# Kernel tuning notes

Hardware: AMD Instinct MI355X
Metric: run time of the kernel (lower is better)

## Reference

```python
import jax, jax.numpy as jnp
import numpy as np

E = 1024   # embed_size
H = 16     # num_heads
D = E // H # head_dim
B, S = 4, 2048

def setup_inputs() -> dict:
    key = jax.random.key(0)
    ks = jax.random.split(key, 11)
    scale = 1.0 / np.sqrt(E)
    inp = {
        "Q": jax.random.normal(ks[0], (B, S, E), jnp.float32),
        "K": jax.random.normal(ks[1], (B, S, E), jnp.float32),
        "V": jax.random.normal(ks[2], (B, S, E), jnp.float32),
        "Wq": jax.random.uniform(ks[3], (E, E), jnp.float32, -scale, scale),
        "bq": jax.random.uniform(ks[4], (E,), jnp.float32, -scale, scale),
        "Wk": jax.random.uniform(ks[5], (E, E), jnp.float32, -scale, scale),
        "bk": jax.random.uniform(ks[6], (E,), jnp.float32, -scale, scale),
        "Wv": jax.random.uniform(ks[7], (E, E), jnp.float32, -scale, scale),
        "bv": jax.random.uniform(ks[8], (E,), jnp.float32, -scale, scale),
        "Wo": jax.random.uniform(ks[9], (E, E), jnp.float32, -scale, scale),
        "bo": jax.random.uniform(ks[10], (E,), jnp.float32, -scale, scale),
    }
    return inp

def reference(Q, K, V, Wq, bq, Wk, bk, Wv, bv, Wo, bo):
    b, sq, _ = Q.shape
    sk = K.shape[1]
    # Linear projections (torch Linear: x @ W.T + b), split into heads -> (b, H, s, D)
    q = (Q @ Wq.T + bq).reshape(b, sq, H, D).transpose(0, 2, 1, 3)
    k = (K @ Wk.T + bk).reshape(b, sk, H, D).transpose(0, 2, 1, 3)
    v = (V @ Wv.T + bv).reshape(b, sk, H, D).transpose(0, 2, 1, 3)
    scores = jnp.einsum('bhqd,bhkd->bhqk', q, k) / jnp.sqrt(jnp.float32(D))
    attn = jax.nn.softmax(scores, axis=-1)
    out = jnp.einsum('bhqk,bhkd->bhqd', attn, v)  # (b, H, sq, D)
    concat = out.transpose(0, 2, 1, 3).reshape(b, sq, E)
    return concat @ Wo.T + bo
```

## Files before the change

### kernel.cpp

```cpp
#include <hip/hip_runtime.h>
#include <hip/hip_bf16.h>

typedef unsigned short u16;
typedef unsigned int u32;
typedef __bf16 bf16x8 __attribute__((ext_vector_type(8)));
typedef float f32x4 __attribute__((ext_vector_type(4)));
typedef float f32x16 __attribute__((ext_vector_type(16)));
typedef unsigned int u32x2 __attribute__((ext_vector_type(2)));

constexpr int E_ = 1024, H_ = 16, D_ = 64, B_ = 4, S_ = 2048;
constexpr int GM = B_ * S_;
constexpr int GN = E_;
constexpr int GK = E_;

__device__ __forceinline__ u16 f2bf(float f) {
  union { float f; u32 u; } v; v.f = f;
  u32 r = v.u + 0x7fffu + ((v.u >> 16) & 1u);
  return (u16)(r >> 16);
}

__device__ __forceinline__ bf16x8 ld_bf16x8(const u16* p) {
  return *reinterpret_cast<const bf16x8*>(p);
}

__device__ __forceinline__ f32x4 mfma16(bf16x8 a, bf16x8 b, f32x4 c) {
  return __builtin_amdgcn_mfma_f32_16x16x32_bf16(a, b, c, 0, 0, 0);
}
__device__ __forceinline__ f32x16 mfma32(bf16x8 a, bf16x8 b, f32x16 c) {
  return __builtin_amdgcn_mfma_f32_32x32x16_bf16(a, b, c, 0, 0, 0);
}

__device__ __forceinline__ u32 cvtpk(float lo, float hi) {
  u32 r;
  asm("v_cvt_pk_bf16_f32 %0, %1, %2" : "=v"(r) : "v"(lo), "v"(hi));
  return r;
}

__device__ __forceinline__ void pl32swap(u32& a, u32& b) {
#if __has_builtin(__builtin_amdgcn_permlane32_swap)
  u32x2 r = __builtin_amdgcn_permlane32_swap(a, b, false, false);
  a = r.x; b = r.y;
#else
  asm volatile("v_permlane32_swap_b32 %0, %1" : "+v"(a), "+v"(b));
#endif
}

__device__ __forceinline__ float fexp2(float x) {
#if __has_builtin(__builtin_amdgcn_exp2f)
  return __builtin_amdgcn_exp2f(x);
#else
  return exp2f(x);
#endif
}

#define GLOAD_LDS16(gp, lp)                                                       \
  __builtin_amdgcn_global_load_lds(                                               \
      (const __attribute__((address_space(1))) u32*)(const void*)(gp),            \
      (__attribute__((address_space(3))) u32*)(void*)(lp), 16, 0, 0)

__global__ __launch_bounds__(256) void cvt7(
    const float4* __restrict__ s0, const float4* __restrict__ s1,
    const float4* __restrict__ s2, const float4* __restrict__ s3,
    const float4* __restrict__ s4, const float4* __restrict__ s5,
    const float4* __restrict__ s6,
    ushort4* __restrict__ d0, ushort4* __restrict__ d1,
    ushort4* __restrict__ d2, ushort4* __restrict__ d3,
    ushort4* __restrict__ d4, ushort4* __restrict__ d5,
    ushort4* __restrict__ d6) {
  long i = (long)blockIdx.x * 256 + threadIdx.x;
  const float4* s; ushort4* d; long j;
  if (i < 2097152L)      { s = s0; d = d0; j = i; }
  else if (i < 4194304L) { s = s1; d = d1; j = i - 2097152L; }
  else if (i < 6291456L) { s = s2; d = d2; j = i - 4194304L; }
  else if (i < 6553600L) { s = s3; d = d3; j = i - 6291456L; }
  else if (i < 6815744L) { s = s4; d = d4; j = i - 6553600L; }
  else if (i < 7077888L) { s = s5; d = d5; j = i - 6815744L; }
  else                   { s = s6; d = d6; j = i - 7077888L; }
  float4 v = s[j];
  ushort4 o;
  o.x = f2bf(v.x); o.y = f2bf(v.y); o.z = f2bf(v.z); o.w = f2bf(v.w);
  d[j] = o;
}

template <int MODE>
__global__ __launch_bounds__(256, 2) void gemm_bt(
    const u16* __restrict__ A, const u16* __restrict__ Bw,
    const float* __restrict__ bias, void* __restrict__ Cout, float scale) {
  __shared__ u16 As[128 * 32];
  __shared__ u16 Bs[128 * 32];
  const int tid = threadIdx.x;
  const int lane = tid & 63, w = tid >> 6;
  const int lr = lane & 15, lg = lane >> 4;
  const int bn = blockIdx.x, bm = blockIdx.y;
  const int wm = (w >> 1) * 64, wn = (w & 1) * 64;

  f32x4 acc[4][4] = {};

  const int byte0 = (w * 2 + 0) * 1024 + lane * 16;
  const int byte1 = (w * 2 + 1) * 1024 + lane * 16;
  const int r0 = byte0 >> 6, c0 = (byte0 & 63) >> 1;
  const int r1 = byte1 >> 6, c1 = (byte1 & 63) >> 1;
  const u16* Arow0 = A + (size_t)(bm * 128 + r0) * GK + c0;
  const u16* Arow1 = A + (size_t)(bm * 128 + r1) * GK + c1;
  const u16* Brow0 = Bw + (size_t)(bn * 128 + r0) * GK + c0;
  const u16* Brow1 = Bw + (size_t)(bn * 128 + r1) * GK + c1;
  u16* As0 = &As[(w * 2 + 0) * 512];
  u16* As1 = &As[(w * 2 + 1) * 512];
  u16* Bs0 = &Bs[(w * 2 + 0) * 512];
  u16* Bs1 = &Bs[(w * 2 + 1) * 512];

  for (int kt = 0; kt < GK / 32; ++kt) {
    const int ko = kt * 32;
    GLOAD_LDS16(Arow0 + ko, As0);
    GLOAD_LDS16(Arow1 + ko, As1);
    GLOAD_LDS16(Brow0 + ko, Bs0);
    GLOAD_LDS16(Brow1 + ko, Bs1);
    __syncthreads();
    bf16x8 af[4], bf_[4];
#pragma unroll
    for (int mi = 0; mi < 4; ++mi)
      af[mi] = ld_bf16x8(&As[(wm + mi * 16 + lr) * 32 + lg * 8]);
#pragma unroll
    for (int ni = 0; ni < 4; ++ni)
      bf_[ni] = ld_bf16x8(&Bs[(wn + ni * 16 + lr) * 32 + lg * 8]);
#pragma unroll
    for (int mi = 0; mi < 4; ++mi)
#pragma unroll
      for (int ni = 0; ni < 4; ++ni)
        acc[mi][ni] = mfma16(af[mi], bf_[ni], acc[mi][ni]);
    __syncthreads();
  }

#pragma unroll
  for (int mi = 0; mi < 4; ++mi)
#pragma unroll
    for (int ni = 0; ni < 4; ++ni) {
      const int n = bn * 128 + wn + ni * 16 + lr;
      const float bv = bias[n];
#pragma unroll
      for (int r = 0; r < 4; ++r) {
        const int m = bm * 128 + wm + mi * 16 + lg * 4 + r;
        const float vv = (acc[mi][ni][r] + bv) * scale;
        if (MODE == 0) {
          const int b = m >> 11, s = m & 2047, h = n >> 6, d = n & 63;
          ((u16*)Cout)[(((size_t)(b * 16 + h) * 2048 + s) * 64) + d] = f2bf(vv);
        } else if (MODE == 1) {
          const int b = m >> 11, s = m & 2047, h = n >> 6, d = n & 63;
          ((u16*)Cout)[((size_t)(b * 16 + h) * 64 + d) * 2048 + s] = f2bf(vv);
        } else {
          ((float*)Cout)[(size_t)m * 1024 + n] = vv;
        }
      }
    }
}

__global__ __launch_bounds__(256, 2) void attn5(
    const u16* __restrict__ q, const u16* __restrict__ k,
    const u16* __restrict__ vT, u16* __restrict__ concat) {
  __shared__ u16 KT[2][64 * 64];
  __shared__ u16 VTl[2][64 * 64];
  const int tid = threadIdx.x, lane = tid & 63, w = tid >> 6;
  const int l31 = lane & 31, hi = lane >> 5;
  const int bid = blockIdx.x;
  const int flat = (bid & 7) * 64 + (bid >> 3);
  const int bh = flat >> 3, qt = flat & 7;
  const u16* qbp = q + (size_t)bh * S_ * D_;
  const char* kbase = (const char*)(k + (size_t)bh * S_ * D_);
  const char* vbase = (const char*)(vT + (size_t)bh * D_ * S_);
  const int q0 = qt * 256 + w * 64;

  bf16x8 qf[2][4];
#pragma unroll
  for (int qs = 0; qs < 2; ++qs)
#pragma unroll
    for (int kc = 0; kc < 4; ++kc)
      qf[qs][kc] =
          ld_bf16x8(&qbp[(size_t)(q0 + qs * 32 + l31) * 64 + kc * 16 + hi * 8]);

  f32x16 acc[2][2] = {};
  float l_[2] = {0.f, 0.f};

  const int srow = w * 8 + (lane >> 3);
  const int cswz = (((lane & 7) ^ (lane >> 3)) << 4);
  const char* gk0 = kbase + (size_t)srow * 128 + cswz;
  const char* gk1 = kbase + (size_t)(32 + srow) * 128 + cswz;
  const char* gv0 = vbase + (size_t)srow * (S_ * 2) + cswz;
  const char* gv1 = vbase + (size_t)(32 + srow) * (S_ * 2) + cswz;

  int col4[4];
#pragma unroll
  for (int c = 0; c < 4; ++c)
    col4[c] = (((c * 32 + hi * 16) ^ ((lane & 7) << 4)) >> 1);
  const int rrow = l31 * 64;

#define STAGE(t, buf)                                                     \
  do {                                                                    \
    GLOAD_LDS16(gk0 + (size_t)(t) * 8192, &KT[buf][(0 * 4 + w) * 512]);   \
    GLOAD_LDS16(gk1 + (size_t)(t) * 8192, &KT[buf][(1 * 4 + w) * 512]);   \
    GLOAD_LDS16(gv0 + (size_t)(t) * 128, &VTl[buf][(0 * 4 + w) * 512]);   \
    GLOAD_LDS16(gv1 + (size_t)(t) * 128, &VTl[buf][(1 * 4 + w) * 512]);   \
  } while (0)

  STAGE(0, 0);
  asm volatile("s_waitcnt vmcnt(0)" ::: "memory");
  __syncthreads();

  for (int t = 0; t < S_ / 64; ++t) {
    const int cur = t & 1, nxt = cur ^ 1;
    if (t < S_ / 64 - 1) STAGE(t + 1, nxt);

    f32x16 sF[2][2] = {};
#pragma unroll
    for (int st = 0; st < 2; ++st)
#pragma unroll
      for (int kc = 0; kc < 4; ++kc) {
        bf16x8 kf = ld_bf16x8(&KT[cur][st * 2048 + rrow + col4[kc]]);
        sF[0][st] = mfma32(kf, qf[0][kc], sF[0][st]);
        sF[1][st] = mfma32(kf, qf[1][kc], sF[1][st]);
      }

    bf16x8 vt[2][4];
#pragma unroll
    for (int ks = 0; ks < 4; ++ks) {
      vt[0][ks] = ld_bf16x8(&VTl[cur][rrow + col4[ks]]);
      vt[1][ks] = ld_bf16x8(&VTl[cur][2048 + rrow + col4[ks]]);
    }

#pragma unroll
    for (int qs = 0; qs < 2; ++qs) {
      float s0 = 0.f, s1 = 0.f, s2 = 0.f, s3 = 0.f;
#pragma unroll
      for (int st = 0; st < 2; ++st)
#pragma unroll
        for (int e = 0; e < 16; e += 4) {
          const float p0 = fexp2(sF[qs][st][e + 0]);
          const float p1 = fexp2(sF[qs][st][e + 1]);
          const float p2 = fexp2(sF[qs][st][e + 2]);
          const float p3 = fexp2(sF[qs][st][e + 3]);
          sF[qs][st][e + 0] = p0; sF[qs][st][e + 1] = p1;
          sF[qs][st][e + 2] = p2; sF[qs][st][e + 3] = p3;
          s0 += p0; s1 += p1; s2 += p2; s3 += p3;
        }
      l_[qs] += (s0 + s1) + (s2 + s3);

#pragma unroll
      for (int ks = 0; ks < 4; ++ks) {
        const int st = ks >> 1, b = (ks & 1) * 8;
        u32 w0 = cvtpk(sF[qs][st][b + 0], sF[qs][st][b + 1]);
        u32 w1 = cvtpk(sF[qs][st][b + 2], sF[qs][st][b + 3]);
        u32 w2 = cvtpk(sF[qs][st][b + 4], sF[qs][st][b + 5]);
        u32 w3 = cvtpk(sF[qs][st][b + 6], sF[qs][st][b + 7]);
        pl32swap(w0, w2);
        pl32swap(w1, w3);
        union { u32 u[4]; bf16x8 v; } pa;
        pa.u[0] = w0; pa.u[1] = w1; pa.u[2] = w2; pa.u[3] = w3;
        acc[qs][0] = mfma32(vt[0][ks], pa.v, acc[qs][0]);
        acc[qs][1] = mfma32(vt[1][ks], pa.v, acc[qs][1]);
      }
    }

    asm volatile("s_waitcnt vmcnt(0)" ::: "memory");
    __syncthreads();
  }
#undef STAGE

  const int b = bh >> 4, h = bh & 15;
#pragma unroll
  for (int qs = 0; qs < 2; ++qs) {
    u32 la = __builtin_bit_cast(u32, l_[qs]), lb = la;
    pl32swap(la, lb);
    const float lt =
        __builtin_bit_cast(float, la) + __builtin_bit_cast(float, lb);
    const float inv = 1.f / lt;
    const int s = q0 + qs * 32 + l31;
    u16* crow = concat + ((size_t)(b * 2048 + s)) * 1024 + h * 64;
#pragma unroll
    for (int dt = 0; dt < 2; ++dt)
#pragma unroll
      for (int g = 0; g < 4; ++g) {
        ushort4 o;
        o.x = f2bf(acc[qs][dt][g * 4 + 0] * inv);
        o.y = f2bf(acc[qs][dt][g * 4 + 1] * inv);
        o.z = f2bf(acc[qs][dt][g * 4 + 2] * inv);
        o.w = f2bf(acc[qs][dt][g * 4 + 3] * inv);
        *(ushort4*)&crow[dt * 32 + g * 8 + hi * 4] = o;
      }
  }
}

extern "C" void kernel_launch(void* const* d_in, const int* in_sizes, int n_in,
                              void* d_out, int out_size, void* d_ws,
                              size_t ws_size, hipStream_t stream) {
  const float* Qf = (const float*)d_in[0];
  const float* Kf = (const float*)d_in[1];
  const float* Vf = (const float*)d_in[2];
  const float* Wq = (const float*)d_in[3];
  const float* bq = (const float*)d_in[4];
  const float* Wk = (const float*)d_in[5];
  const float* bk = (const float*)d_in[6];
  const float* Wv = (const float*)d_in[7];
  const float* bv = (const float*)d_in[8];
  const float* Wo = (const float*)d_in[9];
  const float* bo = (const float*)d_in[10];

  char* ws = (char*)d_ws;
  u16* Xq = (u16*)(ws);
  u16* Xk = Xq + 8388608;
  u16* Xv = Xk + 8388608;
  u16* Wqb = (u16*)(ws + (size_t)3 * 16777216);
  u16* Wkb = Wqb + 1048576;
  u16* Wvb = Wkb + 1048576;
  u16* Wob = Wvb + 1048576;
  u16* qb = (u16*)(ws + (size_t)3 * 16777216 + 8388608);
  u16* kb = qb + (size_t)GM * GN;
  u16* vTb = kb + (size_t)GM * GN;
  u16* concat = Xq;

  cvt7<<<28672, 256, 0, stream>>>(
      (const float4*)Qf, (const float4*)Kf, (const float4*)Vf,
      (const float4*)Wq, (const float4*)Wk, (const float4*)Wv,
      (const float4*)Wo, (ushort4*)Xq, (ushort4*)Xk, (ushort4*)Xv,
      (ushort4*)Wqb, (ushort4*)Wkb, (ushort4*)Wvb, (ushort4*)Wob);

  dim3 gg(GN / 128, GM / 128);
  gemm_bt<0><<<gg, 256, 0, stream>>>(Xq, Wqb, bq, qb, 0.18033688011112042f);
  gemm_bt<0><<<gg, 256, 0, stream>>>(Xk, Wkb, bk, kb, 1.0f);
  gemm_bt<1><<<gg, 256, 0, stream>>>(Xv, Wvb, bv, vTb, 1.0f);

  attn5<<<512, 256, 0, stream>>>(qb, kb, vTb, concat);

  gemm_bt<2><<<gg, 256, 0, stream>>>(concat, Wob, bo, (void*)d_out, 1.0f);
}
```

Before: 221.9 us.

## Double attention block to 8 waves and compute softmax row sums via MFMA

The attention kernel now runs 512 threads per block, with each block covering 512 queries of a head, so each K/V tile staged in shared memory is reused by twice as many waves and global loads per query drop. The exp row-sum moves from scalar adds plus a cross-lane swap onto an extra MFMA against a ones vector, which offloads VALU work to the matrix cores. The cost is half as many blocks (less parallelism across CUs), an extra MFMA per step, and denominators summed from bf16-rounded probabilities.

```diff
diff --git a/kernel.cpp b/kernel.cpp
--- a/kernel.cpp
+++ b/kernel.cpp
@@ -154,7 +154,7 @@
     }
 }
 
-__global__ __launch_bounds__(256, 2) void attn5(
+__global__ __launch_bounds__(512, 2) void attn7(
     const u16* __restrict__ q, const u16* __restrict__ k,
     const u16* __restrict__ vT, u16* __restrict__ concat) {
   __shared__ u16 KT[2][64 * 64];
@@ -162,12 +162,12 @@
   const int tid = threadIdx.x, lane = tid & 63, w = tid >> 6;
   const int l31 = lane & 31, hi = lane >> 5;
   const int bid = blockIdx.x;
-  const int flat = (bid & 7) * 64 + (bid >> 3);
-  const int bh = flat >> 3, qt = flat & 7;
+  const int flat = (bid & 7) * 32 + (bid >> 3);
+  const int bh = flat >> 2, qt = flat & 3;
   const u16* qbp = q + (size_t)bh * S_ * D_;
   const char* kbase = (const char*)(k + (size_t)bh * S_ * D_);
   const char* vbase = (const char*)(vT + (size_t)bh * D_ * S_);
-  const int q0 = qt * 256 + w * 64;
+  const int q0 = qt * 512 + w * 64;
 
   bf16x8 qf[2][4];
 #pragma unroll
@@ -178,14 +178,14 @@
           ld_bf16x8(&qbp[(size_t)(q0 + qs * 32 + l31) * 64 + kc * 16 + hi * 8]);
 
   f32x16 acc[2][2] = {};
-  float l_[2] = {0.f, 0.f};
-
-  const int srow = w * 8 + (lane >> 3);
-  const int cswz = (((lane & 7) ^ (lane >> 3)) << 4);
-  const char* gk0 = kbase + (size_t)srow * 128 + cswz;
-  const char* gk1 = kbase + (size_t)(32 + srow) * 128 + cswz;
-  const char* gv0 = vbase + (size_t)srow * (S_ * 2) + cswz;
-  const char* gv1 = vbase + (size_t)(32 + srow) * (S_ * 2) + cswz;
+  f32x16 accl[2] = {};
+  union { u32 u[4]; bf16x8 v; } ones_;
+  ones_.u[0] = ones_.u[1] = ones_.u[2] = ones_.u[3] = 0x3F803F80u;
+
+  const int srow = tid >> 3;
+  const int csw = ((tid & 7) ^ (srow & 7)) << 4;
+  const char* gk = kbase + (size_t)srow * 128 + csw;
+  const char* gv = vbase + (size_t)srow * 4096 + csw;
 
   int col4[4];
 #pragma unroll
@@ -193,12 +193,10 @@
     col4[c] = (((c * 32 + hi * 16) ^ ((lane & 7) << 4)) >> 1);
   const int rrow = l31 * 64;
 
-#define STAGE(t, buf)                                                     \
-  do {                                                                    \
-    GLOAD_LDS16(gk0 + (size_t)(t) * 8192, &KT[buf][(0 * 4 + w) * 512]);   \
-    GLOAD_LDS16(gk1 + (size_t)(t) * 8192, &KT[buf][(1 * 4 + w) * 512]);   \
-    GLOAD_LDS16(gv0 + (size_t)(t) * 128, &VTl[buf][(0 * 4 + w) * 512]);   \
-    GLOAD_LDS16(gv1 + (size_t)(t) * 128, &VTl[buf][(1 * 4 + w) * 512]);   \
+#define STAGE(t, buf)                                            \
+  do {                                                           \
+    GLOAD_LDS16(gk + (size_t)(t) * 8192, &KT[buf][tid * 8]);     \
+    GLOAD_LDS16(gv + (size_t)(t) * 128, &VTl[buf][tid * 8]);     \
   } while (0)
 
   STAGE(0, 0);
@@ -228,20 +226,10 @@
 
 #pragma unroll
     for (int qs = 0; qs < 2; ++qs) {
-      float s0 = 0.f, s1 = 0.f, s2 = 0.f, s3 = 0.f;
 #pragma unroll
       for (int st = 0; st < 2; ++st)
 #pragma unroll
-        for (int e = 0; e < 16; e += 4) {
-          const float p0 = fexp2(sF[qs][st][e + 0]);
-          const float p1 = fexp2(sF[qs][st][e + 1]);
-          const float p2 = fexp2(sF[qs][st][e + 2]);
-          const float p3 = fexp2(sF[qs][st][e + 3]);
-          sF[qs][st][e + 0] = p0; sF[qs][st][e + 1] = p1;
-          sF[qs][st][e + 2] = p2; sF[qs][st][e + 3] = p3;
-          s0 += p0; s1 += p1; s2 += p2; s3 += p3;
-        }
-      l_[qs] += (s0 + s1) + (s2 + s3);
+        for (int e = 0; e < 16; ++e) sF[qs][st][e] = fexp2(sF[qs][st][e]);
 
 #pragma unroll
       for (int ks = 0; ks < 4; ++ks) {
@@ -256,6 +244,7 @@
         pa.u[0] = w0; pa.u[1] = w1; pa.u[2] = w2; pa.u[3] = w3;
         acc[qs][0] = mfma32(vt[0][ks], pa.v, acc[qs][0]);
         acc[qs][1] = mfma32(vt[1][ks], pa.v, acc[qs][1]);
+        accl[qs] = mfma32(ones_.v, pa.v, accl[qs]);
       }
     }
 
@@ -267,11 +256,7 @@
   const int b = bh >> 4, h = bh & 15;
 #pragma unroll
   for (int qs = 0; qs < 2; ++qs) {
-    u32 la = __builtin_bit_cast(u32, l_[qs]), lb = la;
-    pl32swap(la, lb);
-    const float lt =
-        __builtin_bit_cast(float, la) + __builtin_bit_cast(float, lb);
-    const float inv = 1.f / lt;
+    const float inv = 1.f / accl[qs][0];
     const int s = q0 + qs * 32 + l31;
     u16* crow = concat + ((size_t)(b * 2048 + s)) * 1024 + h * 64;
 #pragma unroll
@@ -327,7 +312,7 @@
   gemm_bt<0><<<gg, 256, 0, stream>>>(Xk, Wkb, bk, kb, 1.0f);
   gemm_bt<1><<<gg, 256, 0, stream>>>(Xv, Wvb, bv, vTb, 1.0f);
 
-  attn5<<<512, 256, 0, stream>>>(qb, kb, vTb, concat);
+  attn7<<<256, 512, 0, stream>>>(qb, kb, vTb, concat);
 
   gemm_bt<2><<<gg, 256, 0, stream>>>(concat, Wob, bo, (void*)d_out, 1.0f);
 }
```

New measurement: 222.8 us. No clear change (+0.4%).

## Load K and V tiles directly from global memory, dropping LDS staging

Applied to the files above, without the earlier changes.

The attention kernel stops staging K and V^T tiles through double-buffered shared memory with async global-to-LDS loads and block barriers. Each wave now reads its MFMA operands straight from global memory, relying on L1/L2 caching since all four waves in a block read the same K/V rows. This removes the barriers and the LDS traffic but gives up explicit prefetch overlap and adds redundant global loads per wave.

```diff
diff --git a/kernel.cpp b/kernel.cpp
--- a/kernel.cpp
+++ b/kernel.cpp
@@ -154,19 +154,15 @@
     }
 }
 
-__global__ __launch_bounds__(256, 2) void attn5(
+__global__ __launch_bounds__(256, 2) void attn8(
     const u16* __restrict__ q, const u16* __restrict__ k,
     const u16* __restrict__ vT, u16* __restrict__ concat) {
-  __shared__ u16 KT[2][64 * 64];
-  __shared__ u16 VTl[2][64 * 64];
   const int tid = threadIdx.x, lane = tid & 63, w = tid >> 6;
   const int l31 = lane & 31, hi = lane >> 5;
   const int bid = blockIdx.x;
   const int flat = (bid & 7) * 64 + (bid >> 3);
   const int bh = flat >> 3, qt = flat & 7;
   const u16* qbp = q + (size_t)bh * S_ * D_;
-  const char* kbase = (const char*)(k + (size_t)bh * S_ * D_);
-  const char* vbase = (const char*)(vT + (size_t)bh * D_ * S_);
   const int q0 = qt * 256 + w * 64;
 
   bf16x8 qf[2][4];
@@ -180,41 +176,19 @@
   f32x16 acc[2][2] = {};
   float l_[2] = {0.f, 0.f};
 
-  const int srow = w * 8 + (lane >> 3);
-  const int cswz = (((lane & 7) ^ (lane >> 3)) << 4);
-  const char* gk0 = kbase + (size_t)srow * 128 + cswz;
-  const char* gk1 = kbase + (size_t)(32 + srow) * 128 + cswz;
-  const char* gv0 = vbase + (size_t)srow * (S_ * 2) + cswz;
-  const char* gv1 = vbase + (size_t)(32 + srow) * (S_ * 2) + cswz;
-
-  int col4[4];
-#pragma unroll
-  for (int c = 0; c < 4; ++c)
-    col4[c] = (((c * 32 + hi * 16) ^ ((lane & 7) << 4)) >> 1);
-  const int rrow = l31 * 64;
-
-#define STAGE(t, buf)                                                     \
-  do {                                                                    \
-    GLOAD_LDS16(gk0 + (size_t)(t) * 8192, &KT[buf][(0 * 4 + w) * 512]);   \
-    GLOAD_LDS16(gk1 + (size_t)(t) * 8192, &KT[buf][(1 * 4 + w) * 512]);   \
-    GLOAD_LDS16(gv0 + (size_t)(t) * 128, &VTl[buf][(0 * 4 + w) * 512]);   \
-    GLOAD_LDS16(gv1 + (size_t)(t) * 128, &VTl[buf][(1 * 4 + w) * 512]);   \
-  } while (0)
-
-  STAGE(0, 0);
-  asm volatile("s_waitcnt vmcnt(0)" ::: "memory");
-  __syncthreads();
+  const u16* kEl = k + (size_t)bh * S_ * D_ + l31 * 64 + hi * 8;
+  const u16* vEl = vT + (size_t)bh * D_ * S_ + (size_t)l31 * 2048 + hi * 8;
 
   for (int t = 0; t < S_ / 64; ++t) {
-    const int cur = t & 1, nxt = cur ^ 1;
-    if (t < S_ / 64 - 1) STAGE(t + 1, nxt);
+    const u16* kt_ = kEl + t * 4096;
+    const u16* vt_ = vEl + t * 64;
 
     f32x16 sF[2][2] = {};
 #pragma unroll
     for (int st = 0; st < 2; ++st)
 #pragma unroll
       for (int kc = 0; kc < 4; ++kc) {
-        bf16x8 kf = ld_bf16x8(&KT[cur][st * 2048 + rrow + col4[kc]]);
+        bf16x8 kf = ld_bf16x8(kt_ + st * 2048 + kc * 16);
         sF[0][st] = mfma32(kf, qf[0][kc], sF[0][st]);
         sF[1][st] = mfma32(kf, qf[1][kc], sF[1][st]);
       }
@@ -222,8 +196,8 @@
     bf16x8 vt[2][4];
 #pragma unroll
     for (int ks = 0; ks < 4; ++ks) {
-      vt[0][ks] = ld_bf16x8(&VTl[cur][rrow + col4[ks]]);
-      vt[1][ks] = ld_bf16x8(&VTl[cur][2048 + rrow + col4[ks]]);
+      vt[0][ks] = ld_bf16x8(vt_ + ks * 16);
+      vt[1][ks] = ld_bf16x8(vt_ + 65536 + ks * 16);
     }
 
 #pragma unroll
@@ -258,11 +232,7 @@
         acc[qs][1] = mfma32(vt[1][ks], pa.v, acc[qs][1]);
       }
     }
-
-    asm volatile("s_waitcnt vmcnt(0)" ::: "memory");
-    __syncthreads();
   }
-#undef STAGE
 
   const int b = bh >> 4, h = bh & 15;
 #pragma unroll
@@ -327,7 +297,7 @@
   gemm_bt<0><<<gg, 256, 0, stream>>>(Xk, Wkb, bk, kb, 1.0f);
   gemm_bt<1><<<gg, 256, 0, stream>>>(Xv, Wvb, bv, vTb, 1.0f);
 
-  attn5<<<512, 256, 0, stream>>>(qb, kb, vTb, concat);
+  attn8<<<512, 256, 0, stream>>>(qb, kb, vTb, concat);
 
   gemm_bt<2><<<gg, 256, 0, stream>>>(concat, Wob, bo, (void*)d_out, 1.0f);
 }
```

After: 268.0 us. +20.8%, slower.
